# Performance work log

Measured on AMD Instinct MI355X. Metric: run time of the kernel, lower is better.

Reference implementation:

```python
import jax, jax.numpy as jnp
import numpy as np

N_NODES = 50000
N_EDGES = 800000
NUM_FEAT = 256
HID = 64
N_CLS = 40
N_LAYERS = 2
EPS = 0.3  # residual scale from __init__ eps


def setup_inputs() -> dict:
    key = jax.random.key(0)
    ks = jax.random.split(key, 8)
    x = jax.random.normal(ks[0], (N_NODES, NUM_FEAT), dtype=jnp.float32)
    edge_index = jax.random.randint(ks[1], (2, N_EDGES), 0, N_NODES, dtype=jnp.int64)
    # xavier-normal-ish scaled weights
    W1 = jax.random.normal(ks[2], (HID, NUM_FEAT), dtype=jnp.float32) * (1.414 * (2.0 / (HID + NUM_FEAT)) ** 0.5)
    b1 = jnp.zeros((HID,), dtype=jnp.float32)
    W2 = jax.random.normal(ks[3], (N_CLS, HID), dtype=jnp.float32) * (1.414 * (2.0 / (N_CLS + HID)) ** 0.5)
    b2 = jnp.zeros((N_CLS,), dtype=jnp.float32)
    gate_w = jax.random.normal(ks[4], (N_LAYERS, 2 * HID), dtype=jnp.float32) * (1.414 * (2.0 / (2 * HID + 1)) ** 0.5)
    gate_b = jnp.zeros((N_LAYERS,), dtype=jnp.float32)
    return {"x": x, "edge_index": edge_index, "W1": W1, "b1": b1,
            "W2": W2, "b2": b2, "gate_w": gate_w, "gate_b": gate_b}


def _forward(x, edge_index, W1, b1, W2, b2, gate_w, gate_b):
    row, col = edge_index[0], edge_index[1]  # row = source, col = target (PyG convention)
    n = x.shape[0]
    ones_e = jnp.ones((edge_index.shape[1],), dtype=x.dtype)
    # degree(row) clamped to >=1, then d^{-1/2}
    deg = jnp.clip(jax.ops.segment_sum(ones_e, row, num_segments=n), 1.0)
    nd = deg ** -0.5  # [N]
    # mean-aggregation denominator: incoming-edge counts per target node
    cnt = jnp.clip(jax.ops.segment_sum(ones_e, col, num_segments=n), 1.0)

    # dense input projection (dropout is eval-mode no-op)
    h = jax.nn.relu(x @ W1.T + b1)  # [N, H]
    raw = h

    nd_edge = nd[row] * nd[col]  # [E]
    for l in range(N_LAYERS):
        hr = h[row]  # [E, H] gather (source)
        hc = h[col]  # [E, H] gather (target)
        # gate: Linear(concat([h[row], h[col]])) == h[row]@w_a + h[col]@w_b
        g = jnp.tanh(hr @ gate_w[l, :HID] + hc @ gate_w[l, HID:] + gate_b[l])  # [E]
        norm = g * nd_edge  # [E]
        msg = norm[:, None] * (hc + hr)  # x_i + x_j, [E, H]
        agg = jax.ops.segment_sum(msg, col, num_segments=n) / cnt[:, None]  # scatter-mean
        h = EPS * raw + agg

    logits = h @ W2.T + b2
    return jax.nn.log_softmax(logits, axis=1)


def reference(x, edge_index, W1, b1, W2, b2, gate_w, gate_b):
    return _forward(x, edge_index, W1, b1, W2, b2, gate_w, gate_b)
```

## Files before the change

### kernel.cpp

```cpp
#include <hip/hip_runtime.h>
#include <math.h>

#define N_NODES 50000
#define N_EDGES 800000
#define NFEAT 256
#define HID 64
#define NCLS 40
#define EPS_RES 0.3f
#define ROWSZ 68
#define SCAN_BLOCKS ((N_NODES + 255) / 256)
#define EB 32
#define CHUNK (N_EDGES / EB)
#define NR 4
#define RNG (N_NODES / NR)

typedef unsigned int uint;
typedef unsigned short ushort;

__device__ __forceinline__ float bflo(uint u) { return __uint_as_float(u << 16); }
__device__ __forceinline__ float bfhi(uint u) { return __uint_as_float(u & 0xFFFF0000u); }
__device__ __forceinline__ uint bf16rne(float f) {
    uint u = __float_as_uint(f);
    return (u + 0x7FFFu + ((u >> 16) & 1u)) >> 16;
}
__device__ __forceinline__ uint bf16rne2(float a, float b) {
    return bf16rne(a) | (bf16rne(b) << 16);
}

__global__ __launch_bounds__(256) void hist_kernel(const int* __restrict__ row,
                                                   const int* __restrict__ col,
                                                   int* __restrict__ degM,
                                                   int* __restrict__ cntM,
                                                   int* __restrict__ rank_local) {
    __shared__ int hist[RNG];
    int t = threadIdx.x;
    int chunk = blockIdx.x;
    int lo = blockIdx.y * RNG;
    int side = blockIdx.z;
    for (int j = t; j < RNG; j += 256) hist[j] = 0;
    __syncthreads();
    const int* idx = side ? col : row;
    int e0 = chunk * CHUNK;
    if (side == 0) {
        for (int base = 0; base < CHUNK; base += 1024) {
            int vb[4];
#pragma unroll
            for (int j = 0; j < 4; j++) {
                int i = base + j * 256 + t;
                vb[j] = (i < CHUNK) ? idx[e0 + i] : -1;
            }
#pragma unroll
            for (int j = 0; j < 4; j++) {
                uint v = (uint)(vb[j] - lo);
                if (v < RNG) atomicAdd(&hist[v], 1);
            }
        }
    } else {
        for (int base = 0; base < CHUNK; base += 1024) {
            int vb[4], ib[4];
#pragma unroll
            for (int j = 0; j < 4; j++) {
                int i = base + j * 256 + t;
                ib[j] = i;
                vb[j] = (i < CHUNK) ? idx[e0 + i] : -1;
            }
#pragma unroll
            for (int j = 0; j < 4; j++) {
                uint v = (uint)(vb[j] - lo);
                if (v < RNG) rank_local[e0 + ib[j]] = atomicAdd(&hist[v], 1);
            }
        }
    }
    __syncthreads();
    int* M = side ? cntM : degM;
    for (int j = t; j < RNG; j += 256) M[chunk * N_NODES + lo + j] = hist[j];
}

__device__ __forceinline__ int block_excl_scan_256(int v, int t, int* wsum) {
    int lane = t & 63, w = t >> 6;
    int sv = v;
#pragma unroll
    for (int d = 1; d < 64; d <<= 1) {
        int o = __shfl_up(sv, d);
        if (lane >= d) sv += o;
    }
    if (lane == 63) wsum[w] = sv;
    __syncthreads();
    int add = 0;
    for (int i = 0; i < w; i++) add += wsum[i];
    return sv + add - v;
}

__global__ void scan1_kernel(const int* __restrict__ degM, int* __restrict__ cntM,
                             int* __restrict__ off, int* __restrict__ bsum,
                             float* __restrict__ nd, float* __restrict__ invcnt) {
    __shared__ int wsum[4];
    int t = threadIdx.x;
    int idx = blockIdx.x * 256 + t;
    int v = 0;
    if (idx < N_NODES) {
        int sD = 0;
#pragma unroll
        for (int c = 0; c < EB; c++) sD += degM[c * N_NODES + idx];
        int run = 0;
#pragma unroll
        for (int c = 0; c < EB; c++) {
            int cv = cntM[c * N_NODES + idx];
            cntM[c * N_NODES + idx] = run;
            run += cv;
        }
        v = run;
        if (sD < 1) sD = 1;
        nd[idx] = rsqrtf((float)sD);
        int cc = run; if (cc < 1) cc = 1;
        invcnt[idx] = 1.0f / (float)cc;
    }
    int excl = block_excl_scan_256(v, t, wsum);
    if (idx < N_NODES) off[idx] = excl;
    if (t == 255) bsum[blockIdx.x] = excl + v;
}

__global__ void scan2_kernel(int* __restrict__ bsum) {
    __shared__ int wsum[4];
    int t = threadIdx.x;
    int v = (t < SCAN_BLOCKS) ? bsum[t] : 0;
    int excl = block_excl_scan_256(v, t, wsum);
    if (t < SCAN_BLOCKS) bsum[t] = excl;
}

__global__ void scan3_kernel(int* __restrict__ off, const int* __restrict__ bsum) {
    int t = threadIdx.x;
    int idx = blockIdx.x * 256 + t;
    if (idx < N_NODES) off[idx] += bsum[blockIdx.x];
    if (idx == 0) off[N_NODES] = N_EDGES;
}

__global__ void scatter_kernel(const int* __restrict__ row, const int* __restrict__ col,
                               const int* __restrict__ rank_local, const int* __restrict__ cntM,
                               const int* __restrict__ off, const float* __restrict__ nd,
                               int2* __restrict__ sedge) {
    int e = blockIdx.x * 256 + threadIdx.x;
    int r = row[e], c = col[e];
    int ch = e / CHUNK;
    int p = off[c] + cntM[ch * N_NODES + c] + rank_local[e];
    int2 se;
    se.x = r;
    se.y = __float_as_int(nd[r] * nd[c]);
    sedge[p] = se;
}

__global__ __launch_bounds__(256) void proj_kernel(const float* __restrict__ x,
                                                   const float* __restrict__ W1,
                                                   const float* __restrict__ b1,
                                                   const float* __restrict__ gw,
                                                   float* __restrict__ ha,
                                                   ushort* __restrict__ habf,
                                                   float* __restrict__ y,
                                                   float* __restrict__ z) {
    __shared__ float xs[64 * ROWSZ];
    __shared__ float ws[64 * ROWSZ];
    int t = threadIdx.x;
    int nb = blockIdx.x * 64;
    int lane = t & 63, w = t >> 6;
    int l15 = lane & 15, g = lane >> 4;
    int hbase = 16 * w + 4 * g;
    float acc[4][4];
#pragma unroll
    for (int j = 0; j < 4; j++)
#pragma unroll
        for (int i = 0; i < 4; i++) acc[j][i] = 0.f;

    for (int kc = 0; kc < NFEAT; kc += 64) {
        __syncthreads();
#pragma unroll
        for (int i = 0; i < 4; i++) {
            int idx = t + 256 * i;
            int r_ = idx >> 4;
            int kq = idx & 15;
            int gn = nb + r_;
            float4 v = make_float4(0.f, 0.f, 0.f, 0.f);
            if (gn < N_NODES) v = *(const float4*)(x + (size_t)gn * NFEAT + kc + kq * 4);
            *(float4*)(xs + r_ * ROWSZ + kq * 4) = v;
            float4 wv = *(const float4*)(W1 + (size_t)r_ * NFEAT + kc + kq * 4);
            *(float4*)(ws + r_ * ROWSZ + kq * 4) = wv;
        }
        __syncthreads();
#pragma unroll 4
        for (int k = 0; k < 64; k += 4) {
            float4 a[4], b[4];
#pragma unroll
            for (int j = 0; j < 4; j++) a[j] = *(const float4*)(xs + (l15 + 16 * j) * ROWSZ + k);
#pragma unroll
            for (int i = 0; i < 4; i++) b[i] = *(const float4*)(ws + (hbase + i) * ROWSZ + k);
#pragma unroll
            for (int j = 0; j < 4; j++)
#pragma unroll
                for (int i = 0; i < 4; i++)
                    acc[j][i] += a[j].x * b[i].x + a[j].y * b[i].y + a[j].z * b[i].z + a[j].w * b[i].w;
        }
    }
    float4 bias = *(const float4*)(b1 + hbase);
    float4 wa4 = *(const float4*)(gw + hbase);
    float4 wb4 = *(const float4*)(gw + HID + hbase);
    int slot = w * 4 + g;
    __syncthreads();
#pragma unroll
    for (int j = 0; j < 4; j++) {
        int gn = nb + l15 + 16 * j;
        float4 o;
        o.x = fmaxf(acc[j][0] + bias.x, 0.f);
        o.y = fmaxf(acc[j][1] + bias.y, 0.f);
        o.z = fmaxf(acc[j][2] + bias.z, 0.f);
        o.w = fmaxf(acc[j][3] + bias.w, 0.f);
        if (gn < N_NODES) {
            *(float4*)(ha + (size_t)gn * HID + hbase) = o;
            uint2 pk;
            pk.x = bf16rne2(o.x, o.y);
            pk.y = bf16rne2(o.z, o.w);
            *(uint2*)(habf + (size_t)gn * HID + hbase) = pk;
        }
        xs[(l15 + 16 * j) * 16 + slot] = o.x * wa4.x + o.y * wa4.y + o.z * wa4.z + o.w * wa4.w;
        ws[(l15 + 16 * j) * 16 + slot] = o.x * wb4.x + o.y * wb4.y + o.z * wb4.z + o.w * wb4.w;
    }
    __syncthreads();
    if (t < 64 && nb + t < N_NODES) {
        float sa = 0.f, sb = 0.f;
#pragma unroll
        for (int s = 0; s < 16; s++) { sa += xs[t * 16 + s]; sb += ws[t * 16 + s]; }
        y[nb + t] = sa;
        z[nb + t] = sb;
    }
}

__device__ __forceinline__ void agg_core8(const ushort* __restrict__ hbf,
                                          const int2* __restrict__ sedge,
                                          const float* __restrict__ y,
                                          float zc_b, int e0, int e1, int q, int c8,
                                          float acc[8], float& gs_out) {
#pragma unroll
    for (int i = 0; i < 8; i++) acc[i] = 0.f;
    float gs = 0.f;
    if (e0 < e1) {
        int eA = e0 + q;
        int ecA = (eA < e1) ? eA : e0;
        int2 seA = sedge[ecA];
        float ndeA = (eA < e1) ? __int_as_float(seA.y) : 0.f;
        int eB = e0 + 8 + q;
        int ecB = (eB < e1) ? eB : e0;
        int2 seB = sedge[ecB];
        float ndeB = (eB < e1) ? __int_as_float(seB.y) : 0.f;
        float yA = y[seA.x];
        uint4 uA = *(const uint4*)(hbf + (size_t)seA.x * HID + c8);
        for (int base = e0; base < e1; base += 8) {
            float yB = y[seB.x];
            uint4 uB = *(const uint4*)(hbf + (size_t)seB.x * HID + c8);
            int eC = base + 16 + q;
            int ecC = (eC < e1) ? eC : e0;
            int2 seC = sedge[ecC];
            float ndeC = (eC < e1) ? __int_as_float(seC.y) : 0.f;
            float gv = tanhf(yA + zc_b) * ndeA;
            acc[0] += gv * bflo(uA.x);
            acc[1] += gv * bfhi(uA.x);
            acc[2] += gv * bflo(uA.y);
            acc[3] += gv * bfhi(uA.y);
            acc[4] += gv * bflo(uA.z);
            acc[5] += gv * bfhi(uA.z);
            acc[6] += gv * bflo(uA.w);
            acc[7] += gv * bfhi(uA.w);
            gs += gv;
            yA = yB; uA = uB; ndeA = ndeB;
            seB = seC; ndeB = ndeC;
        }
    }
#pragma unroll
    for (int s = 8; s < 64; s <<= 1) {
#pragma unroll
        for (int i = 0; i < 8; i++) acc[i] += __shfl_xor(acc[i], s);
        gs += __shfl_xor(gs, s);
    }
    gs_out = gs;
}

__global__ void agg1_kernel(const float* __restrict__ ha, const ushort* __restrict__ habf,
                            const int2* __restrict__ sedge, const int* __restrict__ off,
                            const float* __restrict__ invcnt, const float* __restrict__ y,
                            const float* __restrict__ z, const float* __restrict__ gb,
                            const float* __restrict__ gw2, ushort* __restrict__ hbbf,
                            float* __restrict__ y2, float* __restrict__ z2) {
    int t = threadIdx.x;
    int lane = t & 63;
    int node = blockIdx.x * 4 + (t >> 6);
    int q = lane >> 3, c8 = (lane & 7) * 8;
    float4 ra = *(const float4*)(ha + (size_t)node * HID + c8);
    float4 rb = *(const float4*)(ha + (size_t)node * HID + c8 + 4);
    float raw8[8] = {ra.x, ra.y, ra.z, ra.w, rb.x, rb.y, rb.z, rb.w};
    float zc_b = z[node] + gb[0];
    float acc[8]; float gs;
    agg_core8(habf, sedge, y, zc_b, off[node], off[node + 1], q, c8, acc, gs);
    float invc = invcnt[node];
    float o[8];
#pragma unroll
    for (int i = 0; i < 8; i++) o[i] = EPS_RES * raw8[i] + (acc[i] + gs * raw8[i]) * invc;
    if (q == 0) {
        uint4 pk;
        pk.x = bf16rne2(o[0], o[1]);
        pk.y = bf16rne2(o[2], o[3]);
        pk.z = bf16rne2(o[4], o[5]);
        pk.w = bf16rne2(o[6], o[7]);
        *(uint4*)(hbbf + (size_t)node * HID + c8) = pk;
    }
    float4 wa0 = *(const float4*)(gw2 + c8);
    float4 wa1 = *(const float4*)(gw2 + c8 + 4);
    float4 wb0 = *(const float4*)(gw2 + HID + c8);
    float4 wb1 = *(const float4*)(gw2 + HID + c8 + 4);
    float p = o[0] * wa0.x + o[1] * wa0.y + o[2] * wa0.z + o[3] * wa0.w
            + o[4] * wa1.x + o[5] * wa1.y + o[6] * wa1.z + o[7] * wa1.w;
    float qq = o[0] * wb0.x + o[1] * wb0.y + o[2] * wb0.z + o[3] * wb0.w
             + o[4] * wb1.x + o[5] * wb1.y + o[6] * wb1.z + o[7] * wb1.w;
#pragma unroll
    for (int s = 1; s < 8; s <<= 1) { p += __shfl_xor(p, s); qq += __shfl_xor(qq, s); }
    if (lane == 0) { y2[node] = p; z2[node] = qq; }
}

__global__ void agg2_kernel(const ushort* __restrict__ hbbf, const float* __restrict__ ha,
                            const int2* __restrict__ sedge, const int* __restrict__ off,
                            const float* __restrict__ invcnt, const float* __restrict__ y2,
                            const float* __restrict__ z2, const float* __restrict__ gb,
                            const float* __restrict__ W2, const float* __restrict__ b2,
                            float* __restrict__ out) {
    __shared__ float w2s[NCLS * 65];
    __shared__ float b2s[NCLS];
    __shared__ float hs[4 * HID];
    int t = threadIdx.x;
    for (int i = t; i < NCLS * HID; i += 256) w2s[(i >> 6) * 65 + (i & 63)] = W2[i];
    if (t < NCLS) b2s[t] = b2[t];
    int lane = t & 63;
    int wv = t >> 6;
    int node = blockIdx.x * 4 + wv;
    int q = lane >> 3, c8 = (lane & 7) * 8;
    uint4 hc = *(const uint4*)(hbbf + (size_t)node * HID + c8);
    float hcv[8] = {bflo(hc.x), bfhi(hc.x), bflo(hc.y), bfhi(hc.y),
                    bflo(hc.z), bfhi(hc.z), bflo(hc.w), bfhi(hc.w)};
    float4 ra = *(const float4*)(ha + (size_t)node * HID + c8);
    float4 rb = *(const float4*)(ha + (size_t)node * HID + c8 + 4);
    float raw8[8] = {ra.x, ra.y, ra.z, ra.w, rb.x, rb.y, rb.z, rb.w};
    float zc_b = z2[node] + gb[0];
    float acc[8]; float gs;
    agg_core8(hbbf, sedge, y2, zc_b, off[node], off[node + 1], q, c8, acc, gs);
    float invc = invcnt[node];
    if (q == 0) {
        float4 o0, o1;
        o0.x = EPS_RES * raw8[0] + (acc[0] + gs * hcv[0]) * invc;
        o0.y = EPS_RES * raw8[1] + (acc[1] + gs * hcv[1]) * invc;
        o0.z = EPS_RES * raw8[2] + (acc[2] + gs * hcv[2]) * invc;
        o0.w = EPS_RES * raw8[3] + (acc[3] + gs * hcv[3]) * invc;
        o1.x = EPS_RES * raw8[4] + (acc[4] + gs * hcv[4]) * invc;
        o1.y = EPS_RES * raw8[5] + (acc[5] + gs * hcv[5]) * invc;
        o1.z = EPS_RES * raw8[6] + (acc[6] + gs * hcv[6]) * invc;
        o1.w = EPS_RES * raw8[7] + (acc[7] + gs * hcv[7]) * invc;
        *(float4*)(hs + wv * HID + c8) = o0;
        *(float4*)(hs + wv * HID + c8 + 4) = o1;
    }
    __syncthreads();
    float logit = 0.f;
    if (lane < NCLS) {
        const float* wr = w2s + lane * 65;
        const float* hrow = hs + wv * HID;
#pragma unroll
        for (int k = 0; k < HID; k++) logit += hrow[k] * wr[k];
        logit += b2s[lane];
    }
    float v = (lane < NCLS) ? logit : -INFINITY;
#pragma unroll
    for (int s = 1; s < 64; s <<= 1) v = fmaxf(v, __shfl_xor(v, s));
    float ex = (lane < NCLS) ? expf(logit - v) : 0.f;
#pragma unroll
    for (int s = 1; s < 64; s <<= 1) ex += __shfl_xor(ex, s);
    float ls = v + logf(ex);
    if (lane < NCLS) out[node * NCLS + lane] = logit - ls;
}

extern "C" void kernel_launch(void* const* d_in, const int* in_sizes, int n_in,
                              void* d_out, int out_size, void* d_ws, size_t ws_size,
                              hipStream_t stream) {
    const float* x  = (const float*)d_in[0];
    const int*   ei = (const int*)d_in[1];
    const float* W1 = (const float*)d_in[2];
    const float* b1 = (const float*)d_in[3];
    const float* W2 = (const float*)d_in[4];
    const float* b2 = (const float*)d_in[5];
    const float* gw = (const float*)d_in[6];
    const float* gb = (const float*)d_in[7];
    float* out = (float*)d_out;

    int2*  sedge  = (int2*)d_ws;
    float* nd     = (float*)(sedge + N_EDGES);
    float* invcnt = nd + N_NODES;
    float* y      = invcnt + N_NODES;
    float* z      = y + N_NODES;
    float* y2     = z + N_NODES;
    float* z2     = y2 + N_NODES;
    float* ha     = z2 + N_NODES;
    ushort* habf  = (ushort*)(ha + (size_t)N_NODES * HID);
    ushort* hbbf  = habf + (size_t)N_NODES * HID;
    int*   off    = (int*)(hbbf + (size_t)N_NODES * HID);
    int*   bsum   = off + N_NODES + 1;
    int*   degM   = (int*)ha;
    int*   cntM   = degM + (size_t)EB * N_NODES;
    int*   rank_local = (int*)habf;

    const int* row = ei;
    const int* col = ei + N_EDGES;

    hist_kernel<<<dim3(EB, NR, 2), 256, 0, stream>>>(row, col, degM, cntM, rank_local);
    scan1_kernel<<<SCAN_BLOCKS, 256, 0, stream>>>(degM, cntM, off, bsum, nd, invcnt);
    scan2_kernel<<<1, 256, 0, stream>>>(bsum);
    scan3_kernel<<<SCAN_BLOCKS, 256, 0, stream>>>(off, bsum);
    scatter_kernel<<<N_EDGES / 256, 256, 0, stream>>>(row, col, rank_local, cntM, off, nd, sedge);
    proj_kernel<<<(N_NODES + 63) / 64, 256, 0, stream>>>(x, W1, b1, gw, ha, habf, y, z);

    agg1_kernel<<<N_NODES / 4, 256, 0, stream>>>(ha, habf, sedge, off, invcnt, y, z, gb,
                                                 gw + 2 * HID, hbbf, y2, z2);
    agg2_kernel<<<N_NODES / 4, 256, 0, stream>>>(hbbf, ha, sedge, off, invcnt, y2, z2,
                                                 gb + 1, W2, b2, out);
}
```

Before: 268.3 us.

## Deepen gather prefetch, use fast tanh, compute logits via readlane broadcasts

The edge aggregation loop now prefetches one more stage of neighbor feature rows and gate scalars, so more gathers are in flight per lane. The libm tanhf is replaced with an exp2/reciprocal approximation. The final classifier no longer stages the new hidden vector in shared memory: each lane reads weights as float4 from a padded shared W2 table and pulls the hidden values straight from registers with readlane. The changes add register pressure, a slight precision loss in tanh, and wasted lanes past 40 classes.

```diff
diff --git a/kernel.cpp b/kernel.cpp
--- a/kernel.cpp
+++ b/kernel.cpp
@@ -25,6 +25,11 @@
 }
 __device__ __forceinline__ uint bf16rne2(float a, float b) {
     return bf16rne(a) | (bf16rne(b) << 16);
+}
+
+__device__ __forceinline__ float fast_tanh(float x) {
+    float t = __builtin_amdgcn_exp2f(x * 2.885390081777927f);
+    return 1.0f - 2.0f * __builtin_amdgcn_rcpf(t + 1.0f);
 }
 
 __global__ __launch_bounds__(256) void hist_kernel(const int* __restrict__ row,
@@ -249,16 +254,22 @@
         int ecB = (eB < e1) ? eB : e0;
         int2 seB = sedge[ecB];
         float ndeB = (eB < e1) ? __int_as_float(seB.y) : 0.f;
+        int eC = e0 + 16 + q;
+        int ecC = (eC < e1) ? eC : e0;
+        int2 seC = sedge[ecC];
+        float ndeC = (eC < e1) ? __int_as_float(seC.y) : 0.f;
         float yA = y[seA.x];
         uint4 uA = *(const uint4*)(hbf + (size_t)seA.x * HID + c8);
+        float yB = y[seB.x];
+        uint4 uB = *(const uint4*)(hbf + (size_t)seB.x * HID + c8);
         for (int base = e0; base < e1; base += 8) {
-            float yB = y[seB.x];
-            uint4 uB = *(const uint4*)(hbf + (size_t)seB.x * HID + c8);
-            int eC = base + 16 + q;
-            int ecC = (eC < e1) ? eC : e0;
-            int2 seC = sedge[ecC];
-            float ndeC = (eC < e1) ? __int_as_float(seC.y) : 0.f;
-            float gv = tanhf(yA + zc_b) * ndeA;
+            float yC = y[seC.x];
+            uint4 uC = *(const uint4*)(hbf + (size_t)seC.x * HID + c8);
+            int eD = base + 24 + q;
+            int ecD = (eD < e1) ? eD : e0;
+            int2 seD = sedge[ecD];
+            float ndeD = (eD < e1) ? __int_as_float(seD.y) : 0.f;
+            float gv = fast_tanh(yA + zc_b) * ndeA;
             acc[0] += gv * bflo(uA.x);
             acc[1] += gv * bfhi(uA.x);
             acc[2] += gv * bflo(uA.y);
@@ -269,7 +280,8 @@
             acc[7] += gv * bfhi(uA.w);
             gs += gv;
             yA = yB; uA = uB; ndeA = ndeB;
-            seB = seC; ndeB = ndeC;
+            yB = yC; uB = uC; ndeB = ndeC;
+            seC = seD; ndeC = ndeD;
         }
     }
 #pragma unroll
@@ -328,11 +340,10 @@
                             const float* __restrict__ z2, const float* __restrict__ gb,
                             const float* __restrict__ W2, const float* __restrict__ b2,
                             float* __restrict__ out) {
-    __shared__ float w2s[NCLS * 65];
+    __shared__ float w2s[64 * 68];
     __shared__ float b2s[NCLS];
-    __shared__ float hs[4 * HID];
-    int t = threadIdx.x;
-    for (int i = t; i < NCLS * HID; i += 256) w2s[(i >> 6) * 65 + (i & 63)] = W2[i];
+    int t = threadIdx.x;
+    for (int i = t; i < NCLS * HID; i += 256) w2s[(i >> 6) * 68 + (i & 63)] = W2[i];
     if (t < NCLS) b2s[t] = b2[t];
     int lane = t & 63;
     int wv = t >> 6;
@@ -348,28 +359,26 @@
     float acc[8]; float gs;
     agg_core8(hbbf, sedge, y2, zc_b, off[node], off[node + 1], q, c8, acc, gs);
     float invc = invcnt[node];
-    if (q == 0) {
-        float4 o0, o1;
-        o0.x = EPS_RES * raw8[0] + (acc[0] + gs * hcv[0]) * invc;
-        o0.y = EPS_RES * raw8[1] + (acc[1] + gs * hcv[1]) * invc;
-        o0.z = EPS_RES * raw8[2] + (acc[2] + gs * hcv[2]) * invc;
-        o0.w = EPS_RES * raw8[3] + (acc[3] + gs * hcv[3]) * invc;
-        o1.x = EPS_RES * raw8[4] + (acc[4] + gs * hcv[4]) * invc;
-        o1.y = EPS_RES * raw8[5] + (acc[5] + gs * hcv[5]) * invc;
-        o1.z = EPS_RES * raw8[6] + (acc[6] + gs * hcv[6]) * invc;
-        o1.w = EPS_RES * raw8[7] + (acc[7] + gs * hcv[7]) * invc;
-        *(float4*)(hs + wv * HID + c8) = o0;
-        *(float4*)(hs + wv * HID + c8 + 4) = o1;
-    }
+    float o[8];
+#pragma unroll
+    for (int i = 0; i < 8; i++) o[i] = EPS_RES * raw8[i] + (acc[i] + gs * hcv[i]) * invc;
     __syncthreads();
     float logit = 0.f;
-    if (lane < NCLS) {
-        const float* wr = w2s + lane * 65;
-        const float* hrow = hs + wv * HID;
-#pragma unroll
-        for (int k = 0; k < HID; k++) logit += hrow[k] * wr[k];
-        logit += b2s[lane];
-    }
+    const float* wr = w2s + lane * 68;
+#pragma unroll
+    for (int g = 0; g < 8; g++) {
+        float4 w0 = *(const float4*)(wr + g * 8);
+        float4 w1 = *(const float4*)(wr + g * 8 + 4);
+        logit += w0.x * __int_as_float(__builtin_amdgcn_readlane(__float_as_int(o[0]), g))
+               + w0.y * __int_as_float(__builtin_amdgcn_readlane(__float_as_int(o[1]), g))
+               + w0.z * __int_as_float(__builtin_amdgcn_readlane(__float_as_int(o[2]), g))
+               + w0.w * __int_as_float(__builtin_amdgcn_readlane(__float_as_int(o[3]), g))
+               + w1.x * __int_as_float(__builtin_amdgcn_readlane(__float_as_int(o[4]), g))
+               + w1.y * __int_as_float(__builtin_amdgcn_readlane(__float_as_int(o[5]), g))
+               + w1.z * __int_as_float(__builtin_amdgcn_readlane(__float_as_int(o[6]), g))
+               + w1.w * __int_as_float(__builtin_amdgcn_readlane(__float_as_int(o[7]), g));
+    }
+    if (lane < NCLS) logit += b2s[lane];
     float v = (lane < NCLS) ? logit : -INFINITY;
 #pragma unroll
     for (int s = 1; s < 64; s <<= 1) v = fmaxf(v, __shfl_xor(v, s));
```

Measured after the change: 262.9 us. 1.02x faster.

## Map one node per 8-lane group in aggregation kernels with fast tanh

Applied to the files above, without the earlier changes.

The aggregation kernels now give each node an 8-lane group instead of a full 64-lane wave, so a block covers 32 nodes. Each group walks its own edge list with a three-deep prefetch, which removes the cross-lane reduction across edge slots. The trip count is the maximum degree across the wave, so lanes with short edge lists idle on skewed degrees. Library tanhf is replaced by an exp2/rcp approximation and log-softmax by hardware exp2/log, at a small accuracy cost. The classifier is restructured so all 8 lanes of a group compute 5 logits each from padded shared memory.

```diff
diff --git a/kernel.cpp b/kernel.cpp
--- a/kernel.cpp
+++ b/kernel.cpp
@@ -25,6 +25,11 @@
 }
 __device__ __forceinline__ uint bf16rne2(float a, float b) {
     return bf16rne(a) | (bf16rne(b) << 16);
+}
+
+__device__ __forceinline__ float fast_tanh(float x) {
+    float t = __builtin_amdgcn_exp2f(x * 2.885390081777927f);
+    return 1.0f - 2.0f * __builtin_amdgcn_rcpf(t + 1.0f);
 }
 
 __global__ __launch_bounds__(256) void hist_kernel(const int* __restrict__ row,
@@ -232,33 +237,36 @@
     }
 }
 
-__device__ __forceinline__ void agg_core8(const ushort* __restrict__ hbf,
-                                          const int2* __restrict__ sedge,
-                                          const float* __restrict__ y,
-                                          float zc_b, int e0, int e1, int q, int c8,
-                                          float acc[8], float& gs_out) {
+__device__ __forceinline__ void agg_group8(const ushort* __restrict__ hbf,
+                                           const int2* __restrict__ sedge,
+                                           const float* __restrict__ yv,
+                                           float zc, int e0, int d, int c8,
+                                           float acc[8], float& gs_out) {
 #pragma unroll
     for (int i = 0; i < 8; i++) acc[i] = 0.f;
     float gs = 0.f;
-    if (e0 < e1) {
-        int eA = e0 + q;
-        int ecA = (eA < e1) ? eA : e0;
-        int2 seA = sedge[ecA];
-        float ndeA = (eA < e1) ? __int_as_float(seA.y) : 0.f;
-        int eB = e0 + 8 + q;
-        int ecB = (eB < e1) ? eB : e0;
-        int2 seB = sedge[ecB];
-        float ndeB = (eB < e1) ? __int_as_float(seB.y) : 0.f;
-        float yA = y[seA.x];
+    int m = d;
+    m = max(m, __shfl_xor(m, 8));
+    m = max(m, __shfl_xor(m, 16));
+    m = max(m, __shfl_xor(m, 32));
+    if (m > 0) {
+        int2 seA = sedge[(0 < d) ? e0 : 0];
+        float ndeA = (0 < d) ? __int_as_float(seA.y) : 0.f;
+        int2 seB = sedge[(1 < d) ? e0 + 1 : 0];
+        float ndeB = (1 < d) ? __int_as_float(seB.y) : 0.f;
+        int2 seC = sedge[(2 < d) ? e0 + 2 : 0];
+        float ndeC = (2 < d) ? __int_as_float(seC.y) : 0.f;
+        float yA = yv[seA.x];
         uint4 uA = *(const uint4*)(hbf + (size_t)seA.x * HID + c8);
-        for (int base = e0; base < e1; base += 8) {
-            float yB = y[seB.x];
-            uint4 uB = *(const uint4*)(hbf + (size_t)seB.x * HID + c8);
-            int eC = base + 16 + q;
-            int ecC = (eC < e1) ? eC : e0;
-            int2 seC = sedge[ecC];
-            float ndeC = (eC < e1) ? __int_as_float(seC.y) : 0.f;
-            float gv = tanhf(yA + zc_b) * ndeA;
+        float yB = yv[seB.x];
+        uint4 uB = *(const uint4*)(hbf + (size_t)seB.x * HID + c8);
+        for (int k = 0; k < m; ++k) {
+            float yC = yv[seC.x];
+            uint4 uC = *(const uint4*)(hbf + (size_t)seC.x * HID + c8);
+            int kD = k + 3;
+            int2 seD = sedge[(kD < d) ? e0 + kD : 0];
+            float ndeD = (kD < d) ? __int_as_float(seD.y) : 0.f;
+            float gv = fast_tanh(yA + zc) * ndeA;
             acc[0] += gv * bflo(uA.x);
             acc[1] += gv * bfhi(uA.x);
             acc[2] += gv * bflo(uA.y);
@@ -269,45 +277,46 @@
             acc[7] += gv * bfhi(uA.w);
             gs += gv;
             yA = yB; uA = uB; ndeA = ndeB;
-            seB = seC; ndeB = ndeC;
-        }
-    }
-#pragma unroll
-    for (int s = 8; s < 64; s <<= 1) {
-#pragma unroll
-        for (int i = 0; i < 8; i++) acc[i] += __shfl_xor(acc[i], s);
-        gs += __shfl_xor(gs, s);
+            yB = yC; uB = uC; ndeB = ndeC;
+            seC = seD; ndeC = ndeD;
+        }
     }
     gs_out = gs;
 }
 
-__global__ void agg1_kernel(const float* __restrict__ ha, const ushort* __restrict__ habf,
-                            const int2* __restrict__ sedge, const int* __restrict__ off,
-                            const float* __restrict__ invcnt, const float* __restrict__ y,
-                            const float* __restrict__ z, const float* __restrict__ gb,
-                            const float* __restrict__ gw2, ushort* __restrict__ hbbf,
-                            float* __restrict__ y2, float* __restrict__ z2) {
+__global__ __launch_bounds__(256) void agg1_kernel(
+        const float* __restrict__ ha, const ushort* __restrict__ habf,
+        const int2* __restrict__ sedge, const int* __restrict__ off,
+        const float* __restrict__ invcnt, const float* __restrict__ y,
+        const float* __restrict__ z, const float* __restrict__ gb,
+        const float* __restrict__ gw2, ushort* __restrict__ hbbf,
+        float* __restrict__ y2, float* __restrict__ z2) {
     int t = threadIdx.x;
     int lane = t & 63;
-    int node = blockIdx.x * 4 + (t >> 6);
-    int q = lane >> 3, c8 = (lane & 7) * 8;
-    float4 ra = *(const float4*)(ha + (size_t)node * HID + c8);
-    float4 rb = *(const float4*)(ha + (size_t)node * HID + c8 + 4);
+    int ln = t >> 3;
+    int node = blockIdx.x * 32 + ln;
+    int nc = (node < N_NODES) ? node : (N_NODES - 1);
+    int c8 = (lane & 7) * 8;
+    int e0 = off[nc];
+    int e1 = off[nc + 1];
+    int d = (node < N_NODES) ? (e1 - e0) : 0;
+    float zc = z[nc] + gb[0];
+    float acc[8]; float gs;
+    agg_group8(habf, sedge, y, zc, e0, d, c8, acc, gs);
+    float invc = invcnt[nc];
+    float4 ra = *(const float4*)(ha + (size_t)nc * HID + c8);
+    float4 rb = *(const float4*)(ha + (size_t)nc * HID + c8 + 4);
     float raw8[8] = {ra.x, ra.y, ra.z, ra.w, rb.x, rb.y, rb.z, rb.w};
-    float zc_b = z[node] + gb[0];
-    float acc[8]; float gs;
-    agg_core8(habf, sedge, y, zc_b, off[node], off[node + 1], q, c8, acc, gs);
-    float invc = invcnt[node];
     float o[8];
 #pragma unroll
     for (int i = 0; i < 8; i++) o[i] = EPS_RES * raw8[i] + (acc[i] + gs * raw8[i]) * invc;
-    if (q == 0) {
+    if (node < N_NODES) {
         uint4 pk;
         pk.x = bf16rne2(o[0], o[1]);
         pk.y = bf16rne2(o[2], o[3]);
         pk.z = bf16rne2(o[4], o[5]);
         pk.w = bf16rne2(o[6], o[7]);
-        *(uint4*)(hbbf + (size_t)node * HID + c8) = pk;
+        *(uint4*)(hbbf + (size_t)nc * HID + c8) = pk;
     }
     float4 wa0 = *(const float4*)(gw2 + c8);
     float4 wa1 = *(const float4*)(gw2 + c8 + 4);
@@ -319,65 +328,81 @@
              + o[4] * wb1.x + o[5] * wb1.y + o[6] * wb1.z + o[7] * wb1.w;
 #pragma unroll
     for (int s = 1; s < 8; s <<= 1) { p += __shfl_xor(p, s); qq += __shfl_xor(qq, s); }
-    if (lane == 0) { y2[node] = p; z2[node] = qq; }
-}
-
-__global__ void agg2_kernel(const ushort* __restrict__ hbbf, const float* __restrict__ ha,
-                            const int2* __restrict__ sedge, const int* __restrict__ off,
-                            const float* __restrict__ invcnt, const float* __restrict__ y2,
-                            const float* __restrict__ z2, const float* __restrict__ gb,
-                            const float* __restrict__ W2, const float* __restrict__ b2,
-                            float* __restrict__ out) {
-    __shared__ float w2s[NCLS * 65];
+    if ((lane & 7) == 0 && node < N_NODES) { y2[node] = p; z2[node] = qq; }
+}
+
+__global__ __launch_bounds__(256) void agg2_kernel(
+        const ushort* __restrict__ hbbf, const float* __restrict__ ha,
+        const int2* __restrict__ sedge, const int* __restrict__ off,
+        const float* __restrict__ invcnt, const float* __restrict__ y2,
+        const float* __restrict__ z2, const float* __restrict__ gb,
+        const float* __restrict__ W2, const float* __restrict__ b2,
+        float* __restrict__ out) {
+    __shared__ float w2s[NCLS * 72];
     __shared__ float b2s[NCLS];
-    __shared__ float hs[4 * HID];
-    int t = threadIdx.x;
-    for (int i = t; i < NCLS * HID; i += 256) w2s[(i >> 6) * 65 + (i & 63)] = W2[i];
+    __shared__ float hs[32 * 72];
+    int t = threadIdx.x;
+    for (int i = t; i < NCLS * HID; i += 256) w2s[(i >> 6) * 72 + (i & 63)] = W2[i];
     if (t < NCLS) b2s[t] = b2[t];
     int lane = t & 63;
-    int wv = t >> 6;
-    int node = blockIdx.x * 4 + wv;
-    int q = lane >> 3, c8 = (lane & 7) * 8;
-    uint4 hc = *(const uint4*)(hbbf + (size_t)node * HID + c8);
+    int ln = t >> 3;
+    int node = blockIdx.x * 32 + ln;
+    int nc = (node < N_NODES) ? node : (N_NODES - 1);
+    int c8 = (lane & 7) * 8;
+    int e0 = off[nc];
+    int e1 = off[nc + 1];
+    int d = (node < N_NODES) ? (e1 - e0) : 0;
+    float zc = z2[nc] + gb[0];
+    float acc[8]; float gs;
+    agg_group8(hbbf, sedge, y2, zc, e0, d, c8, acc, gs);
+    float invc = invcnt[nc];
+    uint4 hc = *(const uint4*)(hbbf + (size_t)nc * HID + c8);
     float hcv[8] = {bflo(hc.x), bfhi(hc.x), bflo(hc.y), bfhi(hc.y),
                     bflo(hc.z), bfhi(hc.z), bflo(hc.w), bfhi(hc.w)};
-    float4 ra = *(const float4*)(ha + (size_t)node * HID + c8);
-    float4 rb = *(const float4*)(ha + (size_t)node * HID + c8 + 4);
+    float4 ra = *(const float4*)(ha + (size_t)nc * HID + c8);
+    float4 rb = *(const float4*)(ha + (size_t)nc * HID + c8 + 4);
     float raw8[8] = {ra.x, ra.y, ra.z, ra.w, rb.x, rb.y, rb.z, rb.w};
-    float zc_b = z2[node] + gb[0];
-    float acc[8]; float gs;
-    agg_core8(hbbf, sedge, y2, zc_b, off[node], off[node + 1], q, c8, acc, gs);
-    float invc = invcnt[node];
-    if (q == 0) {
-        float4 o0, o1;
-        o0.x = EPS_RES * raw8[0] + (acc[0] + gs * hcv[0]) * invc;
-        o0.y = EPS_RES * raw8[1] + (acc[1] + gs * hcv[1]) * invc;
-        o0.z = EPS_RES * raw8[2] + (acc[2] + gs * hcv[2]) * invc;
-        o0.w = EPS_RES * raw8[3] + (acc[3] + gs * hcv[3]) * invc;
-        o1.x = EPS_RES * raw8[4] + (acc[4] + gs * hcv[4]) * invc;
-        o1.y = EPS_RES * raw8[5] + (acc[5] + gs * hcv[5]) * invc;
-        o1.z = EPS_RES * raw8[6] + (acc[6] + gs * hcv[6]) * invc;
-        o1.w = EPS_RES * raw8[7] + (acc[7] + gs * hcv[7]) * invc;
-        *(float4*)(hs + wv * HID + c8) = o0;
-        *(float4*)(hs + wv * HID + c8 + 4) = o1;
-    }
-    __syncthreads();
-    float logit = 0.f;
-    if (lane < NCLS) {
-        const float* wr = w2s + lane * 65;
-        const float* hrow = hs + wv * HID;
-#pragma unroll
-        for (int k = 0; k < HID; k++) logit += hrow[k] * wr[k];
-        logit += b2s[lane];
-    }
-    float v = (lane < NCLS) ? logit : -INFINITY;
-#pragma unroll
-    for (int s = 1; s < 64; s <<= 1) v = fmaxf(v, __shfl_xor(v, s));
-    float ex = (lane < NCLS) ? expf(logit - v) : 0.f;
-#pragma unroll
-    for (int s = 1; s < 64; s <<= 1) ex += __shfl_xor(ex, s);
-    float ls = v + logf(ex);
-    if (lane < NCLS) out[node * NCLS + lane] = logit - ls;
+    float4 o0, o1;
+    o0.x = EPS_RES * raw8[0] + (acc[0] + gs * hcv[0]) * invc;
+    o0.y = EPS_RES * raw8[1] + (acc[1] + gs * hcv[1]) * invc;
+    o0.z = EPS_RES * raw8[2] + (acc[2] + gs * hcv[2]) * invc;
+    o0.w = EPS_RES * raw8[3] + (acc[3] + gs * hcv[3]) * invc;
+    o1.x = EPS_RES * raw8[4] + (acc[4] + gs * hcv[4]) * invc;
+    o1.y = EPS_RES * raw8[5] + (acc[5] + gs * hcv[5]) * invc;
+    o1.z = EPS_RES * raw8[6] + (acc[6] + gs * hcv[6]) * invc;
+    o1.w = EPS_RES * raw8[7] + (acc[7] + gs * hcv[7]) * invc;
+    *(float4*)(hs + ln * 72 + c8) = o0;
+    *(float4*)(hs + ln * 72 + c8 + 4) = o1;
+    __syncthreads();
+    int k5 = t & 7;
+    float lg[5];
+#pragma unroll
+    for (int j = 0; j < 5; j++) lg[j] = b2s[k5 + 8 * j];
+    const float* hrow = hs + ln * 72;
+#pragma unroll
+    for (int j4 = 0; j4 < 16; j4++) {
+        float4 h4 = *(const float4*)(hrow + j4 * 4);
+#pragma unroll
+        for (int j = 0; j < 5; j++) {
+            float4 w4 = *(const float4*)(w2s + (k5 + 8 * j) * 72 + j4 * 4);
+            lg[j] += h4.x * w4.x + h4.y * w4.y + h4.z * w4.z + h4.w * w4.w;
+        }
+    }
+    float v = fmaxf(fmaxf(fmaxf(lg[0], lg[1]), fmaxf(lg[2], lg[3])), lg[4]);
+    v = fmaxf(v, __shfl_xor(v, 1));
+    v = fmaxf(v, __shfl_xor(v, 2));
+    v = fmaxf(v, __shfl_xor(v, 4));
+    float ex = 0.f;
+#pragma unroll
+    for (int j = 0; j < 5; j++) ex += __builtin_amdgcn_exp2f((lg[j] - v) * 1.44269504088896f);
+    ex += __shfl_xor(ex, 1);
+    ex += __shfl_xor(ex, 2);
+    ex += __shfl_xor(ex, 4);
+    float ls = v + __builtin_amdgcn_logf(ex) * 0.693147180559945f;
+    if (node < N_NODES) {
+#pragma unroll
+        for (int j = 0; j < 5; j++) out[(size_t)node * NCLS + k5 + 8 * j] = lg[j] - ls;
+    }
 }
 
 extern "C" void kernel_launch(void* const* d_in, const int* in_sizes, int n_in,
@@ -419,8 +444,9 @@
     scatter_kernel<<<N_EDGES / 256, 256, 0, stream>>>(row, col, rank_local, cntM, off, nd, sedge);
     proj_kernel<<<(N_NODES + 63) / 64, 256, 0, stream>>>(x, W1, b1, gw, ha, habf, y, z);
 
-    agg1_kernel<<<N_NODES / 4, 256, 0, stream>>>(ha, habf, sedge, off, invcnt, y, z, gb,
-                                                 gw + 2 * HID, hbbf, y2, z2);
-    agg2_kernel<<<N_NODES / 4, 256, 0, stream>>>(hbbf, ha, sedge, off, invcnt, y2, z2,
-                                                 gb + 1, W2, b2, out);
-}
+    int aggblocks = (N_NODES + 31) / 32;
+    agg1_kernel<<<aggblocks, 256, 0, stream>>>(ha, habf, sedge, off, invcnt, y, z, gb,
+                                               gw + 2 * HID, hbbf, y2, z2);
+    agg2_kernel<<<aggblocks, 256, 0, stream>>>(hbbf, ha, sedge, off, invcnt, y2, z2,
+                                               gb + 1, W2, b2, out);
+}
```

Result: faster. 235.3 us (-12.3%).
